# Kernel optimization log

Measured on AMD Instinct MI355X. Metric: run time of the kernel, lower is better.

Reference implementation:

```python
import jax, jax.numpy as jnp
import numpy as np

EMBED_DIM = 1024
NUM_HEADS = 16
HEAD_DIM = EMBED_DIM // NUM_HEADS


def setup_inputs() -> dict:
    key = jax.random.key(0)
    ks = jax.random.split(key, 11)
    B, S, D = 4, 2048, EMBED_DIM
    s = 1.0 / np.sqrt(D)
    return {
        "q": jax.random.normal(ks[0], (B, S, D), jnp.float32),
        "k": jax.random.normal(ks[1], (B, S, D), jnp.float32),
        "v": jax.random.normal(ks[2], (B, S, D), jnp.float32),
        "Wq": jax.random.normal(ks[3], (D, D), jnp.float32) * s,
        "bq": jnp.zeros((D,), jnp.float32),
        "Wk": jax.random.normal(ks[4], (D, D), jnp.float32) * s,
        "bk": jnp.zeros((D,), jnp.float32),
        "Wv": jax.random.normal(ks[5], (D, D), jnp.float32) * s,
        "bv": jnp.zeros((D,), jnp.float32),
        "Wo": jax.random.normal(ks[6], (D, D), jnp.float32) * s,
        "bo": jnp.zeros((D,), jnp.float32),
    }


def reference(q, k, v, Wq, bq, Wk, bk, Wv, bv, Wo, bo):
    B, S, D = q.shape
    H, Hd = NUM_HEADS, HEAD_DIM
    # projections, split heads -> [B, H, S, Hd]
    qh = (q @ Wq + bq).reshape(B, S, H, Hd).transpose(0, 2, 1, 3)
    kh = (k @ Wk + bk).reshape(B, S, H, Hd).transpose(0, 2, 1, 3)
    vh = (v @ Wv + bv).reshape(B, S, H, Hd).transpose(0, 2, 1, 3)
    scale = 1.0 / jnp.sqrt(jnp.asarray(Hd, qh.dtype))
    scores = jnp.einsum('bhqd,bhkd->bhqk', qh, kh) * scale  # [B,H,S,S]
    attn = jax.nn.softmax(scores, axis=-1)  # dropout = identity in eval
    out = jnp.einsum('bhqk,bhkd->bhqd', attn, vh)
    out = out.transpose(0, 2, 1, 3).reshape(B, S, D)
    return out @ Wo + bo
```

## Files before the change

### kernel.cpp

```cpp
#include <hip/hip_runtime.h>

typedef __attribute__((ext_vector_type(8))) __bf16 bf16x8;
typedef __attribute__((ext_vector_type(4))) __bf16 bf16x4;
typedef __attribute__((ext_vector_type(4))) float f32x4;
typedef __attribute__((ext_vector_type(16))) float f32x16;
typedef __attribute__((ext_vector_type(4))) unsigned int u32x4;

#define GLDS(g, l) __builtin_amdgcn_global_load_lds( \
    (const __attribute__((address_space(1))) void*)(g), \
    (__attribute__((address_space(3))) void*)(l), 16, 0, 0)

__device__ __forceinline__ unsigned cvtpk_bf16(float lo, float hi) {
    unsigned r;
    asm("v_cvt_pk_bf16_f32 %0, %1, %2" : "=v"(r) : "v"(lo), "v"(hi));
    return r;
}
__device__ __forceinline__ void pl32swap(unsigned& a, unsigned& b) {
    asm("v_permlane32_swap_b32 %0, %1" : "+v"(a), "+v"(b));
}

__global__ __launch_bounds__(256) void cvt_tile(const float* __restrict__ q,
                                                const float* __restrict__ k,
                                                const float* __restrict__ v,
                                                __bf16* __restrict__ qo,
                                                __bf16* __restrict__ ko,
                                                __bf16* __restrict__ vo) {
    const float* src = blockIdx.z == 0 ? q : blockIdx.z == 1 ? k : v;
    __bf16* dst = blockIdx.z == 0 ? qo : blockIdx.z == 1 ? ko : vo;
    __shared__ __align__(16) __bf16 sb[128 * 64];
    const int t = threadIdx.x;
    const int m0 = blockIdx.x * 128, kk0 = blockIdx.y * 64;
    #pragma unroll
    for (int i = 0; i < 4; i++) {
        int cid = i * 256 + t;
        int r = cid >> 3, cc = cid & 7;
        const float* p = src + (size_t)(m0 + r) * 1024 + kk0 + cc * 8;
        float4 a = *(const float4*)p;
        float4 b2 = *(const float4*)(p + 4);
        bf16x8 o;
        o[0] = (__bf16)a.x;  o[1] = (__bf16)a.y;  o[2] = (__bf16)a.z;  o[3] = (__bf16)a.w;
        o[4] = (__bf16)b2.x; o[5] = (__bf16)b2.y; o[6] = (__bf16)b2.z; o[7] = (__bf16)b2.w;
        *(bf16x8*)((char*)sb + r * 128 + ((cc ^ (r & 7)) << 4)) = o;
    }
    __syncthreads();
    const int mt = blockIdx.x >> 1, rowbase = (blockIdx.x & 1) * 128;
    #pragma unroll
    for (int i = 0; i < 4; i++) {
        int cid = i * 256 + t;
        int ch = cid >> 7, r = cid & 127;
        bf16x8 o = *(const bf16x8*)((const char*)sb + r * 128 + ((ch ^ (r & 7)) << 4));
        size_t off = (size_t)mt * 262144 + (size_t)blockIdx.y * 16384
                   + (size_t)ch * 2048 + (size_t)(rowbase + r) * 8;
        *(bf16x8*)(dst + off) = o;
    }
}

__global__ __launch_bounds__(256) void wtrans2(const float* __restrict__ W0,
                                               const float* __restrict__ W1,
                                               const float* __restrict__ W2,
                                               const float* __restrict__ W3,
                                               __bf16* __restrict__ O0,
                                               __bf16* __restrict__ O1,
                                               __bf16* __restrict__ O2,
                                               __bf16* __restrict__ O3) {
    const int z = blockIdx.z;
    const float* W = z == 0 ? W0 : z == 1 ? W1 : z == 2 ? W2 : W3;
    __bf16* Wt2 = z == 0 ? O0 : z == 1 ? O1 : z == 2 ? O2 : O3;
    __shared__ float lw[64][65];
    const int kt = blockIdx.y * 64, nt = blockIdx.x * 64;
    const int t = threadIdx.x;
    const int r = t >> 4;
    const int c4 = (t & 15) * 4;
    #pragma unroll
    for (int rr = 0; rr < 64; rr += 16) {
        float4 vv = *(const float4*)&W[(size_t)(kt + r + rr) * 1024 + nt + c4];
        lw[r + rr][c4 + 0] = vv.x; lw[r + rr][c4 + 1] = vv.y;
        lw[r + rr][c4 + 2] = vv.z; lw[r + rr][c4 + 3] = vv.w;
    }
    __syncthreads();
    #pragma unroll
    for (int rr = 0; rr < 64; rr += 16) {
        int n = nt + r + rr;
        bf16x4 ov;
        #pragma unroll
        for (int i = 0; i < 4; i++) ov[i] = (__bf16)lw[c4 + i][r + rr];
        int kg = kt + c4;
        size_t off = (size_t)(n >> 7) * 131072 + (size_t)(kg >> 6) * 8192
                   + (size_t)((kg >> 3) & 7) * 1024 + (size_t)(n & 127) * 8 + (kg & 7);
        *(bf16x4*)&Wt2[off] = ov;
    }
}

template <int QKV>
__global__ __launch_bounds__(512, 2)
void gemm_ph(const __bf16* __restrict__ A0, const __bf16* __restrict__ A1,
             const __bf16* __restrict__ A2,
             const __bf16* __restrict__ B0, const __bf16* __restrict__ B1,
             const __bf16* __restrict__ B2,
             const float* __restrict__ bi0, const float* __restrict__ bi1,
             const float* __restrict__ bi2,
             void* __restrict__ C0, void* __restrict__ C1, void* __restrict__ C2) {
    __shared__ __align__(16) __bf16 sA[3 * 16384];
    __shared__ __align__(16) __bf16 sB[3 * 8192];
    const int t = threadIdx.x, l = t & 63;
    const int wv = t >> 6;
    const int wm = wv >> 1, wn = wv & 1;
    const int y = blockIdx.y;
    const __bf16* At = QKV ? (y == 0 ? A0 : y == 1 ? A1 : A2) : A0;
    const __bf16* Bt = QKV ? (y == 0 ? B0 : y == 1 ? B1 : B2) : B0;
    const float* bias = QKV ? (y == 0 ? bi0 : y == 1 ? bi1 : bi2) : bi0;
    void* Cout        = QKV ? (y == 0 ? C0 : y == 1 ? C1 : C2) : C0;
    const int mode = QKV ? y + 1 : 0;

    const int bid = blockIdx.x;
    const int wgid = (bid & 7) * 32 + (bid >> 3);
    const int mt = wgid >> 3, ntg = wgid & 7;
    const __bf16* Ag = At + (size_t)mt * 262144;
    const __bf16* Bg = Bt + (size_t)ntg * 131072;

    const int aRow = ((wm * 64 + (l & 31)) << 4) + ((l >> 5) << 12);
    const int bRow = ((wn * 64 + (l & 31)) << 4) + ((l >> 5) << 11);

#define STG0(T_, nb_) do { \
    GLDS(Ag + (T_) * 16384 + t * 8,         (char*)sA + (nb_) * 32768 + t * 16); \
    GLDS(Ag + (T_) * 16384 + 4096 + t * 8,  (char*)sA + (nb_) * 32768 + 8192 + t * 16); \
    GLDS(Bg + (T_) * 8192 + t * 8,          (char*)sB + (nb_) * 16384 + t * 16); \
} while (0)
#define STG1(T_, nb_) do { \
    GLDS(Ag + (T_) * 16384 + 8192 + t * 8,  (char*)sA + (nb_) * 32768 + 16384 + t * 16); \
    GLDS(Ag + (T_) * 16384 + 12288 + t * 8, (char*)sA + (nb_) * 32768 + 24576 + t * 16); \
    GLDS(Bg + (T_) * 8192 + 4096 + t * 8,   (char*)sB + (nb_) * 16384 + 8192 + t * 16); \
} while (0)

    f32x16 acc[2][2];
    acc[0][0] = (f32x16){}; acc[0][1] = (f32x16){};
    acc[1][0] = (f32x16){}; acc[1][1] = (f32x16){};

    STG0(0, 0); STG1(0, 0);
    STG0(1, 1); STG1(1, 1);
    asm volatile("s_waitcnt vmcnt(6)" ::: "memory");
    __builtin_amdgcn_s_barrier();

    int cur = 0;
    #pragma unroll 1
    for (int T = 0; T < 16; ++T) {
        const char* bA = (const char*)sA + cur * 32768;
        const char* bB = (const char*)sB + cur * 16384;
        const int nb = cur >= 1 ? cur - 1 : 2;
        #pragma unroll
        for (int ph = 0; ph < 2; ph++) {
            bf16x8 af[2][2], bfr[2][2];
            #pragma unroll
            for (int ks = 0; ks < 2; ks++) {
                int kst = ph * 2 + ks;
                #pragma unroll
                for (int r = 0; r < 2; r++) {
                    af[ks][r]  = *(const bf16x8*)(bA + kst * 8192 + aRow + r * 512);
                    bfr[ks][r] = *(const bf16x8*)(bB + kst * 4096 + bRow + r * 512);
                }
            }
            if (T + 2 < 16) {
                if (ph == 0) STG0(T + 2, nb); else STG1(T + 2, nb);
            }
            __builtin_amdgcn_s_barrier();
            asm volatile("s_waitcnt lgkmcnt(0)" ::: "memory");
            __builtin_amdgcn_sched_barrier(0);
            __builtin_amdgcn_s_setprio(1);
            #pragma unroll
            for (int ks = 0; ks < 2; ks++)
                #pragma unroll
                for (int r = 0; r < 2; r++)
                    #pragma unroll
                    for (int cc = 0; cc < 2; cc++)
                        acc[r][cc] = __builtin_amdgcn_mfma_f32_32x32x16_bf16(
                            af[ks][r], bfr[ks][cc], acc[r][cc], 0, 0, 0);
            __builtin_amdgcn_s_setprio(0);
            if (ph == 1) {
                if (T < 14) asm volatile("s_waitcnt vmcnt(6)" ::: "memory");
                else        asm volatile("s_waitcnt vmcnt(0)" ::: "memory");
            }
            __builtin_amdgcn_s_barrier();
        }
        cur = cur == 2 ? 0 : cur + 1;
    }
#undef STG0
#undef STG1

    const int m0 = mt * 256, col0 = ntg * 128;
    #pragma unroll
    for (int cc = 0; cc < 2; cc++) {
        int col = col0 + wn * 64 + cc * 32 + (l & 31);
        float bv = bias[col];
        #pragma unroll
        for (int r = 0; r < 2; r++) {
            #pragma unroll
            for (int reg = 0; reg < 16; reg++) {
                int row = m0 + wm * 64 + r * 32 + (reg & 3) + 8 * (reg >> 2) + 4 * (l >> 5);
                float vvv = acc[r][cc][reg] + bv;
                if (mode == 0) {
                    ((float*)Cout)[(size_t)row * 1024 + col] = vvv;
                } else if (mode == 1) {
                    ((__bf16*)Cout)[(size_t)row * 1024 + col] = (__bf16)(vvv * 0.18033688f);
                } else if (mode == 2) {
                    int b_ = row >> 11, s_ = row & 2047, h_ = col >> 6, hd_ = col & 63;
                    size_t off = ((size_t)(b_ * 16 + h_) * 32 + (s_ >> 6)) * 4096
                               + (size_t)(hd_ >> 3) * 512 + (s_ & 63) * 8 + (hd_ & 7);
                    ((__bf16*)Cout)[off] = (__bf16)vvv;
                } else {
                    int b_ = row >> 11, s_ = row & 2047, h_ = col >> 6, d_ = col & 63;
                    size_t off = ((size_t)(b_ * 16 + h_) * 32 + (s_ >> 6)) * 4096
                               + (size_t)((s_ & 63) >> 3) * 512 + (size_t)d_ * 8 + (s_ & 7);
                    ((__bf16*)Cout)[off] = (__bf16)vvv;
                }
            }
        }
    }
}

__global__ __launch_bounds__(256, 2)
void attn_fwd(const __bf16* __restrict__ Qp, const __bf16* __restrict__ Kt,
              const __bf16* __restrict__ Vtt, __bf16* __restrict__ AOt) {
    constexpr int S = 2048, D = 1024;
    __shared__ __align__(16) __bf16 sK[3 * 4096];
    __shared__ __align__(16) __bf16 sV[3 * 4096];
    __shared__ float sL[4][64];
    const int t = threadIdx.x, l = t & 63, w = t >> 6;
    const int c = l & 31, g = l >> 5;
    const int bid = blockIdx.x, slot = bid >> 3;
    const int bh = (slot >> 3) * 8 + (bid & 7);
    const int qb = slot & 7;
    const int b = bh >> 4, h = bh & 15;
    const int q0 = qb * 256;
    const __bf16* Kb = Kt + (size_t)bh * 131072;
    const __bf16* Vb = Vtt + (size_t)bh * 131072;

    bf16x8 qf[2][4];
    #pragma unroll
    for (int qh = 0; qh < 2; qh++) {
        const __bf16* qp = Qp + (size_t)(b * S + q0 + w * 64 + qh * 32 + c) * D + h * 64;
        #pragma unroll
        for (int ks = 0; ks < 4; ks++)
            qf[qh][ks] = *(const bf16x8*)(qp + ks * 16 + g * 8);
    }
    asm volatile("s_waitcnt vmcnt(0)" ::: "memory");

#define AISSUE(ti_, buf_) do { \
    GLDS(Kb + (ti_) * 4096 + t * 8,        (char*)sK + (buf_) * 8192 + t * 16); \
    GLDS(Kb + (ti_) * 4096 + 2048 + t * 8, (char*)sK + (buf_) * 8192 + 4096 + t * 16); \
    GLDS(Vb + (ti_) * 4096 + t * 8,        (char*)sV + (buf_) * 8192 + t * 16); \
    GLDS(Vb + (ti_) * 4096 + 2048 + t * 8, (char*)sV + (buf_) * 8192 + 4096 + t * 16); \
} while (0)

    f32x16 acc[2][2];
    acc[0][0] = (f32x16){}; acc[0][1] = (f32x16){};
    acc[1][0] = (f32x16){}; acc[1][1] = (f32x16){};
    float ls[2] = {0.f, 0.f};

    AISSUE(0, 0);
    AISSUE(1, 1);
    int cur = 0;
    #pragma unroll 1
    for (int tile = 0; tile < 32; ++tile) {
        if (tile < 31) asm volatile("s_waitcnt vmcnt(4)" ::: "memory");
        else           asm volatile("s_waitcnt vmcnt(0)" ::: "memory");
        __builtin_amdgcn_s_barrier();
        __builtin_amdgcn_sched_barrier(0);
        const __bf16* bK = sK + cur * 4096;
        const __bf16* bV = sV + cur * 4096;
        #pragma unroll
        for (int kt = 0; kt < 2; kt++) {
            bf16x8 kf[4];
            #pragma unroll
            for (int ks = 0; ks < 4; ks++)
                kf[ks] = *(const bf16x8*)(bK + ((2 * ks + g) * 64 + kt * 32 + c) * 8);
            bf16x8 vq0[2], vq1[2];
            #pragma unroll
            for (int ti = 0; ti < 2; ti++) {
                vq0[ti] = *(const bf16x8*)(bV + ((4 * kt + g) * 64 + ti * 32 + c) * 8);
                vq1[ti] = *(const bf16x8*)(bV + ((4 * kt + 2 + g) * 64 + ti * 32 + c) * 8);
            }
            #pragma unroll
            for (int qh = 0; qh < 2; qh++) {
                f32x16 St = {};
                St = __builtin_amdgcn_mfma_f32_32x32x16_bf16(kf[0], qf[qh][0], St, 0, 0, 0);
                St = __builtin_amdgcn_mfma_f32_32x32x16_bf16(kf[1], qf[qh][1], St, 0, 0, 0);
                St = __builtin_amdgcn_mfma_f32_32x32x16_bf16(kf[2], qf[qh][2], St, 0, 0, 0);
                St = __builtin_amdgcn_mfma_f32_32x32x16_bf16(kf[3], qf[qh][3], St, 0, 0, 0);
                #pragma unroll
                for (int r2 = 0; r2 < 16; r2++) {
                    float p = __builtin_amdgcn_exp2f(St[r2]);
                    ls[qh] += p;
                    St[r2] = p;
                }
                unsigned w0 = cvtpk_bf16(St[0], St[1]),   w1 = cvtpk_bf16(St[2], St[3]);
                unsigned w2 = cvtpk_bf16(St[4], St[5]),   w3 = cvtpk_bf16(St[6], St[7]);
                unsigned w4 = cvtpk_bf16(St[8], St[9]),   w5 = cvtpk_bf16(St[10], St[11]);
                unsigned w6 = cvtpk_bf16(St[12], St[13]), w7 = cvtpk_bf16(St[14], St[15]);
                pl32swap(w0, w2); pl32swap(w1, w3);
                pl32swap(w4, w6); pl32swap(w5, w7);
                bf16x8 pa0 = __builtin_bit_cast(bf16x8, (u32x4){w0, w1, w2, w3});
                bf16x8 pa1 = __builtin_bit_cast(bf16x8, (u32x4){w4, w5, w6, w7});
                acc[qh][0] = __builtin_amdgcn_mfma_f32_32x32x16_bf16(pa0, vq0[0], acc[qh][0], 0, 0, 0);
                acc[qh][1] = __builtin_amdgcn_mfma_f32_32x32x16_bf16(pa0, vq0[1], acc[qh][1], 0, 0, 0);
                acc[qh][0] = __builtin_amdgcn_mfma_f32_32x32x16_bf16(pa1, vq1[0], acc[qh][0], 0, 0, 0);
                acc[qh][1] = __builtin_amdgcn_mfma_f32_32x32x16_bf16(pa1, vq1[1], acc[qh][1], 0, 0, 0);
            }
        }
        if (tile + 2 < 32) AISSUE(tile + 2, cur >= 1 ? cur - 1 : 2);
        cur = cur == 2 ? 0 : cur + 1;
    }
#undef AISSUE

    float tt0 = ls[0] + __shfl_xor(ls[0], 32);
    float tt1 = ls[1] + __shfl_xor(ls[1], 32);
    if (l < 32) { sL[w][l] = 1.0f / tt0; sL[w][32 + l] = 1.0f / tt1; }
    __syncthreads();

    const int mt = b * 8 + qb;
    #pragma unroll
    for (int qh = 0; qh < 2; qh++)
        #pragma unroll
        for (int rq = 0; rq < 4; rq++)
            #pragma unroll
            for (int rr2 = 0; rr2 < 4; rr2++) {
                int reg = rq * 4 + rr2;
                int rloc = rr2 + 8 * rq + 4 * g;
                float rn = sL[w][qh * 32 + rloc];
                int qloc = w * 64 + qh * 32 + rloc;
                size_t base = (size_t)mt * 262144 + (size_t)h * 16384
                            + (size_t)(c >> 3) * 2048 + (size_t)qloc * 8 + (c & 7);
                AOt[base] = (__bf16)(acc[qh][0][reg] * rn);
                AOt[base + 8192] = (__bf16)(acc[qh][1][reg] * rn);
            }
}

extern "C" void kernel_launch(void* const* d_in, const int* in_sizes, int n_in,
                              void* d_out, int out_size, void* d_ws, size_t ws_size,
                              hipStream_t stream) {
    const float* q  = (const float*)d_in[0];
    const float* k  = (const float*)d_in[1];
    const float* v  = (const float*)d_in[2];
    const float* Wq = (const float*)d_in[3];
    const float* bq = (const float*)d_in[4];
    const float* Wk = (const float*)d_in[5];
    const float* bk = (const float*)d_in[6];
    const float* Wv = (const float*)d_in[7];
    const float* bv = (const float*)d_in[8];
    const float* Wo = (const float*)d_in[9];
    const float* bo = (const float*)d_in[10];

    char* ws = (char*)d_ws;
    const size_t MiB = 1024 * 1024;
    __bf16* Atq = (__bf16*)(ws);
    __bf16* Atk = (__bf16*)(ws + 16 * MiB);
    __bf16* Atv = (__bf16*)(ws + 32 * MiB);
    __bf16* W2q = (__bf16*)(ws + 48 * MiB);
    __bf16* W2k = (__bf16*)(ws + 50 * MiB);
    __bf16* W2v = (__bf16*)(ws + 52 * MiB);
    __bf16* W2o = (__bf16*)(ws + 54 * MiB);
    __bf16* Qp  = (__bf16*)(ws + 56 * MiB);
    __bf16* Kt  = (__bf16*)(ws + 72 * MiB);
    __bf16* Vtt = (__bf16*)(ws + 88 * MiB);
    __bf16* AOt = (__bf16*)(ws);

    cvt_tile<<<dim3(64, 16, 3), 256, 0, stream>>>(q, k, v, Atq, Atk, Atv);

    wtrans2<<<dim3(16, 16, 4), 256, 0, stream>>>(Wq, Wk, Wv, Wo, W2q, W2k, W2v, W2o);

    gemm_ph<1><<<dim3(256, 3), 512, 0, stream>>>(Atq, Atk, Atv, W2q, W2k, W2v,
                                                 bq, bk, bv, Qp, Kt, Vtt);

    attn_fwd<<<512, 256, 0, stream>>>(Qp, Kt, Vtt, AOt);

    gemm_ph<0><<<dim3(256, 1), 512, 0, stream>>>(AOt, AOt, AOt, W2o, W2o, W2o,
                                                 bo, bo, bo, d_out, d_out, d_out);
}
```

Baseline: 202.0 us.

## Restructure projection GEMMs to 256-thread blocks with 32-wide K steps

Result: no change. 203.7 us (+0.8%).

```diff
diff --git a/kernel.cpp b/kernel.cpp
--- a/kernel.cpp
+++ b/kernel.cpp
@@ -49,8 +49,8 @@
         int cid = i * 256 + t;
         int ch = cid >> 7, r = cid & 127;
         bf16x8 o = *(const bf16x8*)((const char*)sb + r * 128 + ((ch ^ (r & 7)) << 4));
-        size_t off = (size_t)mt * 262144 + (size_t)blockIdx.y * 16384
-                   + (size_t)ch * 2048 + (size_t)(rowbase + r) * 8;
+        size_t off = (size_t)mt * 262144 + (size_t)(blockIdx.y * 2 + (ch >> 2)) * 8192
+                   + (size_t)(ch & 3) * 2048 + (size_t)(rowbase + r) * 8;
         *(bf16x8*)(dst + off) = o;
     }
 }
@@ -85,24 +85,24 @@
         #pragma unroll
         for (int i = 0; i < 4; i++) ov[i] = (__bf16)lw[c4 + i][r + rr];
         int kg = kt + c4;
-        size_t off = (size_t)(n >> 7) * 131072 + (size_t)(kg >> 6) * 8192
-                   + (size_t)((kg >> 3) & 7) * 1024 + (size_t)(n & 127) * 8 + (kg & 7);
+        size_t off = (size_t)(n >> 7) * 131072 + (size_t)(kg >> 5) * 4096
+                   + (size_t)((kg >> 3) & 3) * 1024 + (size_t)(n & 127) * 8 + (kg & 7);
         *(bf16x4*)&Wt2[off] = ov;
     }
 }
 
 template <int QKV>
-__global__ __launch_bounds__(512, 2)
-void gemm_ph(const __bf16* __restrict__ A0, const __bf16* __restrict__ A1,
-             const __bf16* __restrict__ A2,
-             const __bf16* __restrict__ B0, const __bf16* __restrict__ B1,
-             const __bf16* __restrict__ B2,
-             const float* __restrict__ bi0, const float* __restrict__ bi1,
-             const float* __restrict__ bi2,
-             void* __restrict__ C0, void* __restrict__ C1, void* __restrict__ C2) {
-    __shared__ __align__(16) __bf16 sA[3 * 16384];
-    __shared__ __align__(16) __bf16 sB[3 * 8192];
+__global__ __launch_bounds__(256, 2)
+void gemm32(const __bf16* __restrict__ A0, const __bf16* __restrict__ A1,
+            const __bf16* __restrict__ A2,
+            const __bf16* __restrict__ B0, const __bf16* __restrict__ B1,
+            const __bf16* __restrict__ B2,
+            const float* __restrict__ bi0, const float* __restrict__ bi1,
+            const float* __restrict__ bi2,
+            void* __restrict__ C0, void* __restrict__ C1, void* __restrict__ C2) {
+    __shared__ __align__(16) char smem[3 * 24576];
     const int t = threadIdx.x, l = t & 63;
+    const int g = l >> 5, c = l & 31;
     const int wv = t >> 6;
     const int wm = wv >> 1, wn = wv & 1;
     const int y = blockIdx.y;
@@ -118,85 +118,70 @@
     const __bf16* Ag = At + (size_t)mt * 262144;
     const __bf16* Bg = Bt + (size_t)ntg * 131072;
 
-    const int aRow = ((wm * 64 + (l & 31)) << 4) + ((l >> 5) << 12);
-    const int bRow = ((wn * 64 + (l & 31)) << 4) + ((l >> 5) << 11);
-
-#define STG0(T_, nb_) do { \
-    GLDS(Ag + (T_) * 16384 + t * 8,         (char*)sA + (nb_) * 32768 + t * 16); \
-    GLDS(Ag + (T_) * 16384 + 4096 + t * 8,  (char*)sA + (nb_) * 32768 + 8192 + t * 16); \
-    GLDS(Bg + (T_) * 8192 + t * 8,          (char*)sB + (nb_) * 16384 + t * 16); \
+    const int aOff = (wm * 128 + c) * 16;
+    const int bOff = (wn * 64 + c) * 16;
+
+#define STG(T_, buf_) do { \
+    GLDS(Ag + (T_) * 8192 + t * 8,        smem + (buf_) * 24576 + t * 16); \
+    GLDS(Ag + (T_) * 8192 + 2048 + t * 8, smem + (buf_) * 24576 + 4096 + t * 16); \
+    GLDS(Ag + (T_) * 8192 + 4096 + t * 8, smem + (buf_) * 24576 + 8192 + t * 16); \
+    GLDS(Ag + (T_) * 8192 + 6144 + t * 8, smem + (buf_) * 24576 + 12288 + t * 16); \
+    GLDS(Bg + (T_) * 4096 + t * 8,        smem + (buf_) * 24576 + 16384 + t * 16); \
+    GLDS(Bg + (T_) * 4096 + 2048 + t * 8, smem + (buf_) * 24576 + 20480 + t * 16); \
 } while (0)
-#define STG1(T_, nb_) do { \
-    GLDS(Ag + (T_) * 16384 + 8192 + t * 8,  (char*)sA + (nb_) * 32768 + 16384 + t * 16); \
-    GLDS(Ag + (T_) * 16384 + 12288 + t * 8, (char*)sA + (nb_) * 32768 + 24576 + t * 16); \
-    GLDS(Bg + (T_) * 8192 + 4096 + t * 8,   (char*)sB + (nb_) * 16384 + 8192 + t * 16); \
-} while (0)
-
-    f32x16 acc[2][2];
-    acc[0][0] = (f32x16){}; acc[0][1] = (f32x16){};
-    acc[1][0] = (f32x16){}; acc[1][1] = (f32x16){};
-
-    STG0(0, 0); STG1(0, 0);
-    STG0(1, 1); STG1(1, 1);
-    asm volatile("s_waitcnt vmcnt(6)" ::: "memory");
-    __builtin_amdgcn_s_barrier();
-
+
+    f32x16 acc[4][2];
+    #pragma unroll
+    for (int i = 0; i < 4; i++) {
+        acc[i][0] = (f32x16){}; acc[i][1] = (f32x16){};
+    }
+
+    STG(0, 0);
+    STG(1, 1);
     int cur = 0;
     #pragma unroll 1
-    for (int T = 0; T < 16; ++T) {
-        const char* bA = (const char*)sA + cur * 32768;
-        const char* bB = (const char*)sB + cur * 16384;
+    for (int T = 0; T < 32; ++T) {
+        if (T < 31) asm volatile("s_waitcnt vmcnt(6)" ::: "memory");
+        else        asm volatile("s_waitcnt vmcnt(0)" ::: "memory");
+        __builtin_amdgcn_s_barrier();
+        __builtin_amdgcn_sched_barrier(0);
         const int nb = cur >= 1 ? cur - 1 : 2;
-        #pragma unroll
-        for (int ph = 0; ph < 2; ph++) {
-            bf16x8 af[2][2], bfr[2][2];
-            #pragma unroll
-            for (int ks = 0; ks < 2; ks++) {
-                int kst = ph * 2 + ks;
+        if (T + 2 < 32) STG(T + 2, nb);
+        const char* bA = smem + cur * 24576;
+        const char* bB = bA + 16384;
+        #pragma unroll
+        for (int s = 0; s < 2; s++) {
+            bf16x8 af[4], bfr[2];
+            #pragma unroll
+            for (int fr = 0; fr < 4; fr++)
+                af[fr] = *(const bf16x8*)(bA + (s * 2 + g) * 4096 + aOff + fr * 512);
+            #pragma unroll
+            for (int fc = 0; fc < 2; fc++)
+                bfr[fc] = *(const bf16x8*)(bB + (s * 2 + g) * 2048 + bOff + fc * 512);
+            __builtin_amdgcn_s_setprio(1);
+            #pragma unroll
+            for (int fr = 0; fr < 4; fr++)
                 #pragma unroll
-                for (int r = 0; r < 2; r++) {
-                    af[ks][r]  = *(const bf16x8*)(bA + kst * 8192 + aRow + r * 512);
-                    bfr[ks][r] = *(const bf16x8*)(bB + kst * 4096 + bRow + r * 512);
-                }
-            }
-            if (T + 2 < 16) {
-                if (ph == 0) STG0(T + 2, nb); else STG1(T + 2, nb);
-            }
-            __builtin_amdgcn_s_barrier();
-            asm volatile("s_waitcnt lgkmcnt(0)" ::: "memory");
-            __builtin_amdgcn_sched_barrier(0);
-            __builtin_amdgcn_s_setprio(1);
-            #pragma unroll
-            for (int ks = 0; ks < 2; ks++)
-                #pragma unroll
-                for (int r = 0; r < 2; r++)
-                    #pragma unroll
-                    for (int cc = 0; cc < 2; cc++)
-                        acc[r][cc] = __builtin_amdgcn_mfma_f32_32x32x16_bf16(
-                            af[ks][r], bfr[ks][cc], acc[r][cc], 0, 0, 0);
+                for (int fc = 0; fc < 2; fc++)
+                    acc[fr][fc] = __builtin_amdgcn_mfma_f32_32x32x16_bf16(
+                        af[fr], bfr[fc], acc[fr][fc], 0, 0, 0);
             __builtin_amdgcn_s_setprio(0);
-            if (ph == 1) {
-                if (T < 14) asm volatile("s_waitcnt vmcnt(6)" ::: "memory");
-                else        asm volatile("s_waitcnt vmcnt(0)" ::: "memory");
-            }
-            __builtin_amdgcn_s_barrier();
         }
         cur = cur == 2 ? 0 : cur + 1;
     }
-#undef STG0
-#undef STG1
+#undef STG
 
     const int m0 = mt * 256, col0 = ntg * 128;
     #pragma unroll
-    for (int cc = 0; cc < 2; cc++) {
-        int col = col0 + wn * 64 + cc * 32 + (l & 31);
+    for (int fc = 0; fc < 2; fc++) {
+        int col = col0 + wn * 64 + fc * 32 + c;
         float bv = bias[col];
         #pragma unroll
-        for (int r = 0; r < 2; r++) {
+        for (int fr = 0; fr < 4; fr++) {
             #pragma unroll
             for (int reg = 0; reg < 16; reg++) {
-                int row = m0 + wm * 64 + r * 32 + (reg & 3) + 8 * (reg >> 2) + 4 * (l >> 5);
-                float vvv = acc[r][cc][reg] + bv;
+                int row = m0 + wm * 128 + fr * 32 + (reg & 3) + 8 * (reg >> 2) + 4 * g;
+                float vvv = acc[fr][fc][reg] + bv;
                 if (mode == 0) {
                     ((float*)Cout)[(size_t)row * 1024 + col] = vvv;
                 } else if (mode == 1) {
@@ -327,7 +312,7 @@
                 int rloc = rr2 + 8 * rq + 4 * g;
                 float rn = sL[w][qh * 32 + rloc];
                 int qloc = w * 64 + qh * 32 + rloc;
-                size_t base = (size_t)mt * 262144 + (size_t)h * 16384
+                size_t base = (size_t)mt * 262144 + (size_t)(h * 2) * 8192
                             + (size_t)(c >> 3) * 2048 + (size_t)qloc * 8 + (c & 7);
                 AOt[base] = (__bf16)(acc[qh][0][reg] * rn);
                 AOt[base + 8192] = (__bf16)(acc[qh][1][reg] * rn);
@@ -367,11 +352,11 @@
 
     wtrans2<<<dim3(16, 16, 4), 256, 0, stream>>>(Wq, Wk, Wv, Wo, W2q, W2k, W2v, W2o);
 
-    gemm_ph<1><<<dim3(256, 3), 512, 0, stream>>>(Atq, Atk, Atv, W2q, W2k, W2v,
-                                                 bq, bk, bv, Qp, Kt, Vtt);
+    gemm32<1><<<dim3(256, 3), 256, 0, stream>>>(Atq, Atk, Atv, W2q, W2k, W2v,
+                                                bq, bk, bv, Qp, Kt, Vtt);
 
     attn_fwd<<<512, 256, 0, stream>>>(Qp, Kt, Vtt, AOt);
 
-    gemm_ph<0><<<dim3(256, 1), 512, 0, stream>>>(AOt, AOt, AOt, W2o, W2o, W2o,
-                                                 bo, bo, bo, d_out, d_out, d_out);
-}
+    gemm32<0><<<dim3(256, 1), 256, 0, stream>>>(AOt, AOt, AOt, W2o, W2o, W2o,
+                                                bo, bo, bo, d_out, d_out, d_out);
+}
```
